# Kernel optimization log

Hardware: AMD Instinct MI355X
Metric: run time of the kernel (lower is better)

The kernel has to match this reference:

```python
import jax, jax.numpy as jnp
import numpy as np

B, T, C, H, W = 8, 8, 32, 16, 28
NH, DK = 4, 8                 # n_head, d_k == d_v
RADIUS = [3, 3, 3, 3]
DILATION = [1, 3, 5, 7]
LN_EPS = 1e-5


def setup_inputs() -> dict:
    key = jax.random.key(0)
    ks = jax.random.split(key, 8)
    s = 1.0 / np.sqrt(C).astype(np.float32)
    return {
        "first": jax.random.normal(ks[0], (B, T, C, H, W), jnp.float32),
        "x": jax.random.normal(ks[1], (B, T, C, H, W), jnp.float32),
        "Wq": jax.random.normal(ks[2], (NH * DK, C), jnp.float32) * s,
        "Wk": jax.random.normal(ks[3], (NH * DK, C), jnp.float32) * s,
        "Wv": jax.random.normal(ks[4], (NH * DK, C), jnp.float32) * s,
        "Wo": jax.random.normal(ks[5], (C, NH * DK), jnp.float32) * s,
        "ln_gamma": 1.0 + 0.1 * jax.random.normal(ks[6], (DK, H, W), jnp.float32),
        "ln_beta": 0.1 * jax.random.normal(ks[7], (DK, H, W), jnp.float32),
    }


def _shift(x, dy, dx):
    # out[..., i, j] = x[..., i+dy, j+dx]; zero out-of-bounds. mask: (H, W) valid.
    h, w = x.shape[-2:]
    xs = jnp.roll(x, (-dy, -dx), axis=(-2, -1))
    mh = (jnp.arange(h) + dy >= 0) & (jnp.arange(h) + dy < h)
    mw = (jnp.arange(w) + dx >= 0) & (jnp.arange(w) + dx < w)
    m = mh[:, None] & mw[None, :]
    return jnp.where(m, xs, 0.0), m


def _head_attn(q, k, v, radius, dilation, scale):
    # q,k,v: (b,t,c,h,w). Returns softmaxed scores P (b,t,O*t,h,w) and
    # aggregation T (b,t,c,h,w). Aggregation uses RAW scaled scores (as the repo
    # does: spatial_temporal_aggregation receives M_A_i, not its softmax).
    b, t, c, h, w = q.shape
    scores, vals, masks = [], [], []
    for dy in range(-radius, radius + 1):
        for dx in range(-radius, radius + 1):
            ks, m = _shift(k, dy * dilation, dx * dilation)
            vs, _ = _shift(v, dy * dilation, dx * dilation)
            # score against all source frames s at the shifted spatial location
            scores.append(jnp.einsum('btchw,bschw->btshw', q, ks))
            vals.append(vs)
            masks.append(m)
    A = jnp.stack(scores, axis=2)                      # (b,t,O,s,h,w), O=(2r+1)^2
    M = jnp.stack(masks, axis=0)                       # (O,h,w)
    A = jnp.where(M[None, None, :, None], A / scale, -jnp.inf)
    O = A.shape[2]
    P = jax.nn.softmax(A.reshape(b, t, O * t, h, w), axis=2)
    Wm = jnp.where(M[None, None, :, None], A, 0.0)     # skip invalid (-inf) slots
    V = jnp.stack(vals, axis=0)                        # (O,b,s,c,h,w)
    Tout = jnp.einsum('btoshw,obschw->btchw', Wm, V)
    return P, Tout


def reference(first, x, Wq, Wk, Wv, Wo, ln_gamma, ln_beta):
    b, t, c, h, w = x.shape
    q = jnp.einsum('btchw,oc->btohw', first, Wq).reshape(b, t, NH, DK, h, w)
    k = jnp.einsum('btchw,oc->btohw', x, Wk).reshape(b, t, NH, DK, h, w)
    v = jnp.einsum('btchw,oc->btohw', x, Wv).reshape(b, t, NH, DK, h, w)
    scale = float(np.sqrt(C / NH))
    Ps, Ts = [], []
    for i in range(NH):
        qi = q[:, :, i]
        mu = jnp.mean(qi, axis=(2, 3, 4), keepdims=True)
        var = jnp.var(qi, axis=(2, 3, 4), keepdims=True)
        qi = (qi - mu) / jnp.sqrt(var + LN_EPS) * ln_gamma + ln_beta
        P, Ti = _head_attn(qi, k[:, :, i], v[:, :, i], RADIUS[i], DILATION[i], scale)
        Ps.append(P)
        Ts.append(Ti)
    M_S = jnp.max(jnp.concatenate(Ps, axis=2), axis=2)   # (b,t,h,w)
    M_T = jnp.concatenate(Ts, axis=2)                    # (b,t,NH*DK,h,w)
    out = jnp.einsum('btchw,oc->btohw', M_T, Wo) * M_S[:, :, None]
    return out
```

## Files before the change

### kernel.cpp

```cpp
#include <hip/hip_runtime.h>

#define Bc 8
#define Tc 8
#define Cc 32
#define Hc 16
#define Wc 28
#define NHc 4
#define DKc 8
#define HWc (Hc*Wc)
#define INV_SCALE 0.35355339059327373f
#define LN_EPSc 1e-5f

typedef _Float16 half8  __attribute__((ext_vector_type(8)));
typedef _Float16 half2v __attribute__((ext_vector_type(2)));

union H8 { half8 v; half2v h2[4]; };


__global__ __launch_bounds__(448) void qkv_ln_kernel(
    const float* __restrict__ first, const float* __restrict__ x,
    const float* __restrict__ Wq, const float* __restrict__ Wk,
    const float* __restrict__ Wv,
    const float* __restrict__ gamma, const float* __restrict__ beta,
    half8* __restrict__ Qh, half8* __restrict__ Kh, float* __restrict__ V)
{
    int blk  = blockIdx.x;
    int head = blk >> 6;
    int bt   = blk & 63;
    int t    = bt % Tc;
    int b    = bt / Tc;
    int tid  = threadIdx.x;

    const float* fp = first + (size_t)bt * Cc * HWc + tid;
    const float* xp = x     + (size_t)bt * Cc * HWc + tid;
    float fv[Cc], xv[Cc];
#pragma unroll
    for (int c = 0; c < Cc; ++c) { fv[c] = fp[c*HWc]; xv[c] = xp[c*HWc]; }

    float qv[DKc], kv[DKc], vv[DKc];
#pragma unroll
    for (int dk = 0; dk < DKc; ++dk) {
        int o = head*DKc + dk;
        float aq = 0.f, ak = 0.f, av = 0.f;
#pragma unroll
        for (int c = 0; c < Cc; ++c) {
            aq = fmaf(Wq[o*Cc+c], fv[c], aq);
            ak = fmaf(Wk[o*Cc+c], xv[c], ak);
            av = fmaf(Wv[o*Cc+c], xv[c], av);
        }
        qv[dk] = aq; kv[dk] = ak; vv[dk] = av;
    }

    int bh = b*NHc + head;
    half8 kh;
#pragma unroll
    for (int dk = 0; dk < DKc; ++dk) kh[dk] = (_Float16)kv[dk];
    Kh[((size_t)bh*Tc + t)*HWc + tid] = kh;

    float* vp = V + (((size_t)bh*Tc + t)*HWc + tid)*DKc;
    *(float4*)(vp)   = make_float4(vv[0],vv[1],vv[2],vv[3]);
    *(float4*)(vp+4) = make_float4(vv[4],vv[5],vv[6],vv[7]);

    float s1 = 0.f, s2 = 0.f;
#pragma unroll
    for (int dk = 0; dk < DKc; ++dk) { s1 += qv[dk]; s2 += qv[dk]*qv[dk]; }
#pragma unroll
    for (int off = 32; off >= 1; off >>= 1) {
        s1 += __shfl_down(s1, off, 64);
        s2 += __shfl_down(s2, off, 64);
    }
    __shared__ float r1[8], r2[8];
    int wid = tid >> 6, lane = tid & 63;
    if (lane == 0) { r1[wid] = s1; r2[wid] = s2; }
    __syncthreads();
    float S1 = 0.f, S2 = 0.f;
#pragma unroll
    for (int wv2 = 0; wv2 < 7; ++wv2) { S1 += r1[wv2]; S2 += r2[wv2]; }
    const float invN = 1.f / (float)(DKc * HWc);
    float mu   = S1 * invN;
    float var  = S2 * invN - mu*mu;
    float rstd = rsqrtf(var + LN_EPSc);

    half8 qh;
#pragma unroll
    for (int dk = 0; dk < DKc; ++dk) {
        float gg = gamma[dk*HWc + tid];
        float bb = beta [dk*HWc + tid];
        qh[dk] = (_Float16)(((qv[dk] - mu) * rstd * gg + bb) * INV_SCALE);
    }
    Qh[((size_t)bh*Tc + t)*HWc + tid] = qh;
}

__global__ __launch_bounds__(448, 4) void attn_kernel(
    const half8* __restrict__ Qh, const half8* __restrict__ Kh,
    const float* __restrict__ V,
    half8* __restrict__ Tpart, float2* __restrict__ LMpart)
{
    int blk = blockIdx.x;
    int p   = blk >> 8;
    int i   = blk & 255;
    int b   = i >> 5;
    int ha  = (i >> 4) & 1;
    int s   = (i >> 1) & 7;
    int th  = i & 1;

    int head = p ? (3 - ha) : ha;
    int dil  = 2*head + 1;
    int bh   = b*NHc + head;
    int t0   = th*4;

    int tid = threadIdx.x;
    int w = tid % Wc;
    int h = tid / Wc;

    __shared__ half8  sK [HWc+1];
    __shared__ float4 sV0[HWc+1], sV1[HWc+1];

    sK[tid] = Kh[((size_t)bh*Tc + s)*HWc + tid];
    const float* vp = V + ((size_t)bh*Tc + s)*HWc*DKc;
    sV0[tid] = *(const float4*)(vp + tid*DKc);
    sV1[tid] = *(const float4*)(vp + tid*DKc + 4);
    if (tid == 0) {
        half8 z = {};
        sK[HWc]  = z;
        sV0[HWc] = make_float4(0.f,0.f,0.f,0.f);
        sV1[HWc] = make_float4(0.f,0.f,0.f,0.f);
    }

    H8 q[4];
#pragma unroll
    for (int j = 0; j < 4; ++j)
        q[j].v = Qh[((size_t)bh*Tc + (t0+j))*HWc + tid];

    float4 a0[4], a1[4];
    float l[4], m[4];
#pragma unroll
    for (int j = 0; j < 4; ++j) {
        a0[j] = make_float4(0.f,0.f,0.f,0.f);
        a1[j] = make_float4(0.f,0.f,0.f,0.f);
        l[j] = 0.f; m[j] = -1e30f;
    }

    __syncthreads();

    for (int dy = -3; dy <= 3; ++dy) {
        int hy = h + dy*dil;
        if ((unsigned)hy >= (unsigned)Hc) continue;
        int rowbase = hy*Wc;
#pragma unroll
        for (int dx = -3; dx <= 3; ++dx) {
            int wx = w + dx*dil;
            bool cv = (unsigned)wx < (unsigned)Wc;
            int idx = cv ? (rowbase + wx) : HWc;
            float bias = cv ? 0.f : -1e30f;
            H8 k; k.v = sK[idx];
            float4 v0 = sV0[idx], v1 = sV1[idx];
#pragma unroll
            for (int j = 0; j < 4; ++j) {
                float sc = __builtin_amdgcn_fdot2(q[j].h2[0], k.h2[0],
                           __builtin_amdgcn_fdot2(q[j].h2[1], k.h2[1],
                           __builtin_amdgcn_fdot2(q[j].h2[2], k.h2[2],
                           __builtin_amdgcn_fdot2(q[j].h2[3], k.h2[3],
                                                  0.f, false), false), false), false);
                float msc = sc + bias;
                m[j] = fmaxf(m[j], msc);
                l[j] += __expf(msc);
                a0[j].x = fmaf(sc, v0.x, a0[j].x);
                a0[j].y = fmaf(sc, v0.y, a0[j].y);
                a0[j].z = fmaf(sc, v0.z, a0[j].z);
                a0[j].w = fmaf(sc, v0.w, a0[j].w);
                a1[j].x = fmaf(sc, v1.x, a1[j].x);
                a1[j].y = fmaf(sc, v1.y, a1[j].y);
                a1[j].z = fmaf(sc, v1.z, a1[j].z);
                a1[j].w = fmaf(sc, v1.w, a1[j].w);
            }
        }
    }

    half8*  tp  = Tpart  + (size_t)(bh*Tc + s)*Tc*HWc + tid;
    float2* lmp = LMpart + (size_t)(bh*Tc + s)*Tc*HWc + tid;
#pragma unroll
    for (int j = 0; j < 4; ++j) {
        half8 hv;
        hv[0] = (_Float16)a0[j].x; hv[1] = (_Float16)a0[j].y;
        hv[2] = (_Float16)a0[j].z; hv[3] = (_Float16)a0[j].w;
        hv[4] = (_Float16)a1[j].x; hv[5] = (_Float16)a1[j].y;
        hv[6] = (_Float16)a1[j].z; hv[7] = (_Float16)a1[j].w;
        tp [(t0+j)*HWc] = hv;
        lmp[(t0+j)*HWc] = make_float2(l[j], m[j]);
    }
}

__global__ __launch_bounds__(448) void outproj_kernel(
    const half8* __restrict__ Tpart, const float2* __restrict__ LMpart,
    const float* __restrict__ Wo, float* __restrict__ out)
{
    int blk = blockIdx.x;
    int og  = blk >> 6;
    int bt  = blk & 63;
    int b   = bt >> 3, t = bt & 7;
    int tid = threadIdx.x;

    float mv[Cc];
    float MS = 0.f;
#pragma unroll
    for (int head = 0; head < NHc; ++head) {
        int bh = b*NHc + head;
        float acc[DKc];
#pragma unroll
        for (int j = 0; j < DKc; ++j) acc[j] = 0.f;
        float lsum = 0.f, mmax = -1e30f;
#pragma unroll
        for (int s = 0; s < Tc; ++s) {
            half8 u = Tpart[(size_t)((bh*Tc + s)*Tc + t)*HWc + tid];
#pragma unroll
            for (int j = 0; j < DKc; ++j) acc[j] += (float)u[j];
            float2 lm = LMpart[(size_t)((bh*Tc + s)*Tc + t)*HWc + tid];
            lsum += lm.x; mmax = fmaxf(mmax, lm.y);
        }
#pragma unroll
        for (int j = 0; j < DKc; ++j) mv[head*DKc + j] = acc[j];
        MS = fmaxf(MS, __expf(mmax) / lsum);
    }
#pragma unroll
    for (int i = 0; i < 8; ++i) {
        int o = og*8 + i;
        float a = 0.f;
#pragma unroll
        for (int c = 0; c < Cc; ++c) a = fmaf(Wo[o*Cc+c], mv[c], a);
        out[((size_t)bt*Cc + o)*HWc + tid] = a * MS;
    }
}

extern "C" void kernel_launch(void* const* d_in, const int* in_sizes, int n_in,
                              void* d_out, int out_size, void* d_ws, size_t ws_size,
                              hipStream_t stream) {
    const float* first = (const float*)d_in[0];
    const float* x     = (const float*)d_in[1];
    const float* Wq    = (const float*)d_in[2];
    const float* Wk    = (const float*)d_in[3];
    const float* Wv    = (const float*)d_in[4];
    const float* Wo    = (const float*)d_in[5];
    const float* g     = (const float*)d_in[6];
    const float* bta   = (const float*)d_in[7];
    float* out = (float*)d_out;

    float* ws = (float*)d_ws;
    const size_t N5 = (size_t)Bc*NHc*Tc*HWc*DKc;
    half8*  Qh  = (half8*)ws;
    half8*  Kh  = (half8*)(ws + N5/2);
    float*  V   = ws + N5;
    half8*  Tp  = (half8*)(ws + 2*N5);
    float2* LMp = (float2*)(ws + 6*N5);

    qkv_ln_kernel <<<Bc*Tc*NHc, 448, 0, stream>>>(first, x, Wq, Wk, Wv, g, bta, Qh, Kh, V);
    attn_kernel   <<<512,       448, 0, stream>>>(Qh, Kh, V, Tp, LMp);
    outproj_kernel<<<256,       448, 0, stream>>>(Tp, LMp, Wo, out);
}
```

Before: 113.8 us.

## Store V in fp16 and restructure outproj to avoid redundant partial reductions

V is now written and staged in shared memory as half8 instead of two float4 arrays, halving V traffic and LDS footprint, with a conversion to float per neighbor in the inner loop. The output projection kernel is reorganized so each block handles a quarter of the spatial positions for all 32 output channels. Each thread reduces one head's partials once and shares them via LDS, instead of every output-group block re-reading all Tpart/LMpart data. Risks are fp16 precision loss on V and extra conversion instructions in the hot attention loop.

```diff
diff --git a/kernel.cpp b/kernel.cpp
--- a/kernel.cpp
+++ b/kernel.cpp
@@ -22,7 +22,7 @@
     const float* __restrict__ Wq, const float* __restrict__ Wk,
     const float* __restrict__ Wv,
     const float* __restrict__ gamma, const float* __restrict__ beta,
-    half8* __restrict__ Qh, half8* __restrict__ Kh, float* __restrict__ V)
+    half8* __restrict__ Qh, half8* __restrict__ Kh, half8* __restrict__ Vh)
 {
     int blk  = blockIdx.x;
     int head = blk >> 6;
@@ -52,14 +52,14 @@
     }
 
     int bh = b*NHc + head;
-    half8 kh;
-#pragma unroll
-    for (int dk = 0; dk < DKc; ++dk) kh[dk] = (_Float16)kv[dk];
+    half8 kh, vh;
+#pragma unroll
+    for (int dk = 0; dk < DKc; ++dk) {
+        kh[dk] = (_Float16)kv[dk];
+        vh[dk] = (_Float16)vv[dk];
+    }
     Kh[((size_t)bh*Tc + t)*HWc + tid] = kh;
-
-    float* vp = V + (((size_t)bh*Tc + t)*HWc + tid)*DKc;
-    *(float4*)(vp)   = make_float4(vv[0],vv[1],vv[2],vv[3]);
-    *(float4*)(vp+4) = make_float4(vv[4],vv[5],vv[6],vv[7]);
+    Vh[((size_t)bh*Tc + t)*HWc + tid] = vh;
 
     float s1 = 0.f, s2 = 0.f;
 #pragma unroll
@@ -93,7 +93,7 @@
 
 __global__ __launch_bounds__(448, 4) void attn_kernel(
     const half8* __restrict__ Qh, const half8* __restrict__ Kh,
-    const float* __restrict__ V,
+    const half8* __restrict__ Vh,
     half8* __restrict__ Tpart, float2* __restrict__ LMpart)
 {
     int blk = blockIdx.x;
@@ -113,18 +113,15 @@
     int w = tid % Wc;
     int h = tid / Wc;
 
-    __shared__ half8  sK [HWc+1];
-    __shared__ float4 sV0[HWc+1], sV1[HWc+1];
+    __shared__ half8 sK[HWc+1];
+    __shared__ half8 sV[HWc+1];
 
     sK[tid] = Kh[((size_t)bh*Tc + s)*HWc + tid];
-    const float* vp = V + ((size_t)bh*Tc + s)*HWc*DKc;
-    sV0[tid] = *(const float4*)(vp + tid*DKc);
-    sV1[tid] = *(const float4*)(vp + tid*DKc + 4);
+    sV[tid] = Vh[((size_t)bh*Tc + s)*HWc + tid];
     if (tid == 0) {
         half8 z = {};
-        sK[HWc]  = z;
-        sV0[HWc] = make_float4(0.f,0.f,0.f,0.f);
-        sV1[HWc] = make_float4(0.f,0.f,0.f,0.f);
+        sK[HWc] = z;
+        sV[HWc] = z;
     }
 
     H8 q[4];
@@ -132,12 +129,12 @@
     for (int j = 0; j < 4; ++j)
         q[j].v = Qh[((size_t)bh*Tc + (t0+j))*HWc + tid];
 
-    float4 a0[4], a1[4];
+    float a[4][DKc];
     float l[4], m[4];
 #pragma unroll
     for (int j = 0; j < 4; ++j) {
-        a0[j] = make_float4(0.f,0.f,0.f,0.f);
-        a1[j] = make_float4(0.f,0.f,0.f,0.f);
+#pragma unroll
+        for (int k = 0; k < DKc; ++k) a[j][k] = 0.f;
         l[j] = 0.f; m[j] = -1e30f;
     }
 
@@ -154,7 +151,10 @@
             int idx = cv ? (rowbase + wx) : HWc;
             float bias = cv ? 0.f : -1e30f;
             H8 k; k.v = sK[idx];
-            float4 v0 = sV0[idx], v1 = sV1[idx];
+            H8 vv; vv.v = sV[idx];
+            float vf[DKc];
+#pragma unroll
+            for (int e = 0; e < DKc; ++e) vf[e] = (float)vv.v[e];
 #pragma unroll
             for (int j = 0; j < 4; ++j) {
                 float sc = __builtin_amdgcn_fdot2(q[j].h2[0], k.h2[0],
@@ -165,14 +165,9 @@
                 float msc = sc + bias;
                 m[j] = fmaxf(m[j], msc);
                 l[j] += __expf(msc);
-                a0[j].x = fmaf(sc, v0.x, a0[j].x);
-                a0[j].y = fmaf(sc, v0.y, a0[j].y);
-                a0[j].z = fmaf(sc, v0.z, a0[j].z);
-                a0[j].w = fmaf(sc, v0.w, a0[j].w);
-                a1[j].x = fmaf(sc, v1.x, a1[j].x);
-                a1[j].y = fmaf(sc, v1.y, a1[j].y);
-                a1[j].z = fmaf(sc, v1.z, a1[j].z);
-                a1[j].w = fmaf(sc, v1.w, a1[j].w);
+#pragma unroll
+                for (int e = 0; e < DKc; ++e)
+                    a[j][e] = fmaf(sc, vf[e], a[j][e]);
             }
         }
     }
@@ -182,10 +177,8 @@
 #pragma unroll
     for (int j = 0; j < 4; ++j) {
         half8 hv;
-        hv[0] = (_Float16)a0[j].x; hv[1] = (_Float16)a0[j].y;
-        hv[2] = (_Float16)a0[j].z; hv[3] = (_Float16)a0[j].w;
-        hv[4] = (_Float16)a1[j].x; hv[5] = (_Float16)a1[j].y;
-        hv[6] = (_Float16)a1[j].z; hv[7] = (_Float16)a1[j].w;
+#pragma unroll
+        for (int e = 0; e < DKc; ++e) hv[e] = (_Float16)a[j][e];
         tp [(t0+j)*HWc] = hv;
         lmp[(t0+j)*HWc] = make_float2(l[j], m[j]);
     }
@@ -196,40 +189,53 @@
     const float* __restrict__ Wo, float* __restrict__ out)
 {
     int blk = blockIdx.x;
-    int og  = blk >> 6;
-    int bt  = blk & 63;
+    int hq  = blk & 3;
+    int bt  = blk >> 2;
     int b   = bt >> 3, t = bt & 7;
-    int tid = threadIdx.x;
-
-    float mv[Cc];
-    float MS = 0.f;
-#pragma unroll
-    for (int head = 0; head < NHc; ++head) {
-        int bh = b*NHc + head;
-        float acc[DKc];
-#pragma unroll
-        for (int j = 0; j < DKc; ++j) acc[j] = 0.f;
-        float lsum = 0.f, mmax = -1e30f;
-#pragma unroll
-        for (int s = 0; s < Tc; ++s) {
-            half8 u = Tpart[(size_t)((bh*Tc + s)*Tc + t)*HWc + tid];
-#pragma unroll
-            for (int j = 0; j < DKc; ++j) acc[j] += (float)u[j];
-            float2 lm = LMpart[(size_t)((bh*Tc + s)*Tc + t)*HWc + tid];
-            lsum += lm.x; mmax = fmaxf(mmax, lm.y);
-        }
-#pragma unroll
-        for (int j = 0; j < DKc; ++j) mv[head*DKc + j] = acc[j];
-        MS = fmaxf(MS, __expf(mmax) / lsum);
-    }
-#pragma unroll
-    for (int i = 0; i < 8; ++i) {
-        int o = og*8 + i;
-        float a = 0.f;
-#pragma unroll
-        for (int c = 0; c < Cc; ++c) a = fmaf(Wo[o*Cc+c], mv[c], a);
-        out[((size_t)bt*Cc + o)*HWc + tid] = a * MS;
-    }
+    int u   = threadIdx.x;
+
+    __shared__ float mvs[112][33];
+    __shared__ float ps [112][5];
+
+    int head = u / 112;
+    int hwq  = u % 112;
+    int hw   = hq*112 + hwq;
+    int bh   = b*NHc + head;
+
+    float acc[DKc];
+#pragma unroll
+    for (int j = 0; j < DKc; ++j) acc[j] = 0.f;
+    float lsum = 0.f, mmax = -1e30f;
+#pragma unroll
+    for (int s = 0; s < Tc; ++s) {
+        size_t base = (size_t)((bh*Tc + s)*Tc + t)*HWc + hw;
+        half8 tv = Tpart[base];
+#pragma unroll
+        for (int j = 0; j < DKc; ++j) acc[j] += (float)tv[j];
+        float2 lm = LMpart[base];
+        lsum += lm.x; mmax = fmaxf(mmax, lm.y);
+    }
+#pragma unroll
+    for (int j = 0; j < DKc; ++j) mvs[hwq][head*DKc + j] = acc[j];
+    ps[hwq][head] = __expf(mmax) / lsum;
+    __syncthreads();
+
+    int og = u / 112;
+    float MS = fmaxf(fmaxf(ps[hwq][0], ps[hwq][1]),
+                     fmaxf(ps[hwq][2], ps[hwq][3]));
+    float o8[8];
+#pragma unroll
+    for (int i = 0; i < 8; ++i) o8[i] = 0.f;
+#pragma unroll
+    for (int c = 0; c < Cc; ++c) {
+        float mv = mvs[hwq][c];
+#pragma unroll
+        for (int i = 0; i < 8; ++i)
+            o8[i] = fmaf(Wo[(og*8 + i)*Cc + c], mv, o8[i]);
+    }
+#pragma unroll
+    for (int i = 0; i < 8; ++i)
+        out[((size_t)bt*Cc + og*8 + i)*HWc + hw] = o8[i] * MS;
 }
 
 extern "C" void kernel_launch(void* const* d_in, const int* in_sizes, int n_in,
@@ -249,11 +255,11 @@
     const size_t N5 = (size_t)Bc*NHc*Tc*HWc*DKc;
     half8*  Qh  = (half8*)ws;
     half8*  Kh  = (half8*)(ws + N5/2);
-    float*  V   = ws + N5;
-    half8*  Tp  = (half8*)(ws + 2*N5);
-    float2* LMp = (float2*)(ws + 6*N5);
-
-    qkv_ln_kernel <<<Bc*Tc*NHc, 448, 0, stream>>>(first, x, Wq, Wk, Wv, g, bta, Qh, Kh, V);
-    attn_kernel   <<<512,       448, 0, stream>>>(Qh, Kh, V, Tp, LMp);
+    half8*  Vh  = (half8*)(ws + N5);
+    half8*  Tp  = (half8*)(ws + 3*N5/2);
+    float2* LMp = (float2*)(ws + 3*N5/2 + 4*N5);
+
+    qkv_ln_kernel <<<Bc*Tc*NHc, 448, 0, stream>>>(first, x, Wq, Wk, Wv, g, bta, Qh, Kh, Vh);
+    attn_kernel   <<<512,       448, 0, stream>>>(Qh, Kh, Vh, Tp, LMp);
     outproj_kernel<<<256,       448, 0, stream>>>(Tp, LMp, Wo, out);
 }
```

After: 178.5 us. 56.8% more time.
